# Performance work log

Measured on AMD Instinct MI355X. Metric: run time of the kernel, lower is better.

## Reference

```python
import jax, jax.numpy as jnp
import numpy as np

B, S, D_IN, E = 64, 199, 1024, 256
INNER, K = 512, 4
NH_M, DH_M = 4, 128
NH_S, DH_S = 4, 64
FF_UP = 384
SLSTM_AT = (1, 4)


def layernorm(x, w, eps=1e-5):
    mu = x.mean(-1, keepdims=True)
    var = x.var(-1, keepdims=True)
    return (x - mu) * jax.lax.rsqrt(var + eps) * w


def mh_layernorm(h, w, eps=1e-5):
    # h: (B,S,NH,DH): normalize per head over DH, scale by w (NH*DH,)
    mu = h.mean(-1, keepdims=True)
    var = h.var(-1, keepdims=True)
    hn = (h - mu) * jax.lax.rsqrt(var + eps)
    b, s, nh, dh = h.shape
    return hn.reshape(b, s, nh * dh) * w


def causal_conv(x, w, b):
    # depthwise causal conv; x (B,S,C), w (C,K), b (C,)
    k = w.shape[-1]
    s = x.shape[1]
    xp = jnp.pad(x, ((0, 0), (k - 1, 0), (0, 0)))
    y = sum(xp[:, i:i + s, :] * w[:, i] for i in range(k))
    return y + b


def headwise(x, w):
    # block-diagonal linear (LinearHeadwiseExpand): x (B,S,H*d), w (H,o,d)
    b, s, _ = x.shape
    h, o, d = w.shape
    y = jnp.einsum('bshd,hod->bsho', x.reshape(b, s, h, d), w)
    return y.reshape(b, s, h * o)


def mlstm_parallel(q, k, v, ig, fg):
    # stabilized parallel mLSTM; q,k,v (B,NH,S,DH); ig,fg (B,NH,S)
    s, dh = q.shape[2], q.shape[3]
    logf = jax.nn.log_sigmoid(fg)
    lfc = jnp.cumsum(logf, axis=-1)
    lfc = jnp.concatenate([jnp.zeros_like(lfc[..., :1]), lfc], axis=-1)  # (B,NH,S+1)
    mat = lfc[..., :, None] - lfc[..., None, :]
    mask = jnp.tril(jnp.ones((s + 1, s + 1), dtype=bool))
    mat = jnp.where(mask, mat, -jnp.inf)
    logD = mat[..., 1:, 1:] + ig[..., None, :]            # (B,NH,S,S)
    maxD = jnp.max(logD, axis=-1, keepdims=True)
    Dm = jnp.exp(logD - maxD)
    qk = jnp.einsum('bnsd,bntd->bnst', q, k) / (dh ** 0.5)
    C = qk * Dm
    norm = jnp.maximum(jnp.abs(C.sum(-1, keepdims=True)), jnp.exp(-maxD))
    return jnp.einsum('bnst,bntd->bnsd', C / (norm + 1e-6), v)


def mlstm_layer(x, proj_up, conv_w, conv_b, q_w, k_w, v_w, ig_w, ig_b, fg_w, fg_b, skip, outnorm_w, proj_down):
    b, s, _ = x.shape
    xi = x @ proj_up                                      # (B,S,2*INNER)
    x_m, z = jnp.split(xi, 2, axis=-1)
    xca = jax.nn.silu(causal_conv(x_m, conv_w, conv_b))
    q = headwise(xca, q_w)
    k = headwise(xca, k_w)
    v = headwise(x_m, v_w)
    gate_in = jnp.concatenate([q, k, v], axis=-1)         # (B,S,3*INNER)
    ig = (gate_in @ ig_w.T + ig_b).transpose(0, 2, 1)     # (B,NH,S)
    fg = (gate_in @ fg_w.T + fg_b).transpose(0, 2, 1)
    qh = q.reshape(b, s, NH_M, DH_M).transpose(0, 2, 1, 3)
    kh = k.reshape(b, s, NH_M, DH_M).transpose(0, 2, 1, 3)
    vh = v.reshape(b, s, NH_M, DH_M).transpose(0, 2, 1, 3)
    h = mlstm_parallel(qh, kh, vh, ig, fg)                # (B,NH,S,DH)
    hn = mh_layernorm(h.transpose(0, 2, 1, 3), outnorm_w) # (B,S,INNER)
    h_state = (hn + skip * xca) * jax.nn.silu(z)
    return h_state @ proj_down


def slstm_layer(x, conv_w, conv_b, gate_w, rec_w, bias, gn_w):
    b, s, _ = x.shape
    xc = jax.nn.silu(causal_conv(x, conv_w, conv_b))
    xch = xc.reshape(b, s, NH_S, DH_S)
    xh = x.reshape(b, s, NH_S, DH_S)
    gi = jnp.einsum('bshd,hod->bsho', xch, gate_w[0])
    gf = jnp.einsum('bshd,hod->bsho', xch, gate_w[1])
    gz = jnp.einsum('bshd,hod->bsho', xh, gate_w[2])
    go = jnp.einsum('bshd,hod->bsho', xh, gate_w[3])
    Wx = jnp.stack([gi, gf, gz, go], axis=2)              # (B,S,4,NH,DH)

    def step(carry, wx):
        h, c, n, m = carry
        raw = wx + jnp.einsum('bhd,ghod->bgho', h, rec_w) + bias
        iraw, fraw, zraw, oraw = raw[:, 0], raw[:, 1], raw[:, 2], raw[:, 3]
        logfplusm = m + jax.nn.log_sigmoid(fraw)
        m_new = jnp.maximum(iraw, logfplusm)
        igate = jnp.exp(iraw - m_new)
        fgate = jnp.exp(logfplusm - m_new)
        c_new = fgate * c + igate * jnp.tanh(zraw)
        n_new = fgate * n + igate
        h_new = jax.nn.sigmoid(oraw) * (c_new / n_new)
        return (h_new, c_new, n_new, m_new), h_new

    z0 = jnp.zeros((b, NH_S, DH_S), x.dtype)
    _, ys = jax.lax.scan(step, (z0, z0, z0, z0), jnp.moveaxis(Wx, 1, 0))
    y = jnp.moveaxis(ys, 0, 1)                            # (B,S,NH,DH)
    return mh_layernorm(y, gn_w)


def gated_ffn(x, w_up, w_dn):
    gate, up = jnp.split(x @ w_up, 2, axis=-1)
    return (jax.nn.gelu(gate) * up) @ w_dn


def forward_fn(x, w_down, b_down, m_ln_w, m_proj_up, m_conv_w, m_conv_b, m_q_w, m_k_w, m_v_w,
               m_ig_w, m_ig_b, m_fg_w, m_fg_b, m_skip, m_outnorm_w, m_proj_down,
               s_ln_w, s_conv_w, s_conv_b, s_gate_w, s_rec_w, s_bias, s_gn_w, s_ln2_w,
               s_ffn_up, s_ffn_down, post_ln_w, w_emo, b_emo, w_sen, b_sen):
    h = x @ w_down + b_down                               # (B,S,E)
    mi = si = 0
    for blk in range(7):
        if blk in SLSTM_AT:
            h = h + slstm_layer(layernorm(h, s_ln_w[si]), s_conv_w[si], s_conv_b[si],
                                s_gate_w[si], s_rec_w[si], s_bias[si], s_gn_w[si])
            h = h + gated_ffn(layernorm(h, s_ln2_w[si]), s_ffn_up[si], s_ffn_down[si])
            si += 1
        else:
            h = h + mlstm_layer(layernorm(h, m_ln_w[mi]), m_proj_up[mi], m_conv_w[mi], m_conv_b[mi],
                                m_q_w[mi], m_k_w[mi], m_v_w[mi], m_ig_w[mi], m_ig_b[mi],
                                m_fg_w[mi], m_fg_b[mi], m_skip[mi], m_outnorm_w[mi], m_proj_down[mi])
            mi += 1
    h = jax.nn.selu(layernorm(h, post_ln_w))
    pooled = h.mean(axis=1)                               # (B,E)
    return pooled @ w_emo + b_emo, pooled @ w_sen + b_sen


def setup_inputs() -> dict:
    ks = iter(jax.random.split(jax.random.key(0), 40))
    def p(*shape, s=0.02):
        return jax.random.normal(next(ks), shape, dtype=jnp.float32) * s
    inp = dict(
        x=jax.random.normal(next(ks), (B, S, D_IN), dtype=jnp.float32),
        w_down=p(D_IN, E), b_down=jnp.zeros((E,), jnp.float32),
        m_ln_w=jnp.ones((5, E), jnp.float32),
        m_proj_up=p(5, E, 2 * INNER),
        m_conv_w=p(5, INNER, K), m_conv_b=jnp.zeros((5, INNER), jnp.float32),
        m_q_w=p(5, 128, 4, 4), m_k_w=p(5, 128, 4, 4), m_v_w=p(5, 128, 4, 4),
        m_ig_w=p(5, NH_M, 3 * INNER), m_ig_b=p(5, NH_M, s=0.1),
        m_fg_w=p(5, NH_M, 3 * INNER),
        m_fg_b=jnp.tile(jnp.linspace(3.0, 6.0, NH_M, dtype=jnp.float32), (5, 1)),
        m_skip=jnp.ones((5, INNER), jnp.float32),
        m_outnorm_w=jnp.ones((5, INNER), jnp.float32),
        m_proj_down=p(5, INNER, E),
        s_ln_w=jnp.ones((2, E), jnp.float32),
        s_conv_w=p(2, E, K), s_conv_b=jnp.zeros((2, E), jnp.float32),
        s_gate_w=p(2, 4, NH_S, DH_S, DH_S),
        s_rec_w=p(2, 4, NH_S, DH_S, DH_S),
        s_bias=jnp.zeros((2, 4, NH_S, DH_S), jnp.float32).at[:, 1].set(3.0),
        s_gn_w=jnp.ones((2, E), jnp.float32),
        s_ln2_w=jnp.ones((2, E), jnp.float32),
        s_ffn_up=p(2, E, 2 * FF_UP), s_ffn_down=p(2, FF_UP, E),
        post_ln_w=jnp.ones((E,), jnp.float32),
        w_emo=p(E, 7), b_emo=jnp.zeros((7,), jnp.float32),
        w_sen=p(E, 3), b_sen=jnp.zeros((3,), jnp.float32),
    )
    return inp


def reference(x, w_down, b_down, m_ln_w, m_proj_up, m_conv_w, m_conv_b, m_q_w, m_k_w, m_v_w,
              m_ig_w, m_ig_b, m_fg_w, m_fg_b, m_skip, m_outnorm_w, m_proj_down,
              s_ln_w, s_conv_w, s_conv_b, s_gate_w, s_rec_w, s_bias, s_gn_w, s_ln2_w,
              s_ffn_up, s_ffn_down, post_ln_w, w_emo, b_emo, w_sen, b_sen):
    return forward_fn(x, w_down, b_down, m_ln_w, m_proj_up, m_conv_w, m_conv_b, m_q_w, m_k_w, m_v_w,
                      m_ig_w, m_ig_b, m_fg_w, m_fg_b, m_skip, m_outnorm_w, m_proj_down,
                      s_ln_w, s_conv_w, s_conv_b, s_gate_w, s_rec_w, s_bias, s_gn_w, s_ln2_w,
                      s_ffn_up, s_ffn_down, post_ln_w, w_emo, b_emo, w_sen, b_sen)
```

## Files before the change

### kernel.cpp

```cpp
#include <hip/hip_runtime.h>
#include <hip/hip_bf16.h>
#include <math.h>


#define B_    64
#define S_    199
#define E_    256
#define NTOK  (B_*S_)
#define NQT   13

typedef __attribute__((ext_vector_type(8))) short short8;
typedef __attribute__((ext_vector_type(4))) float floatx4;
typedef unsigned short ushort_t;

__device__ __forceinline__ float sigmoidf_(float x) { return 1.f / (1.f + expf(-x)); }
__device__ __forceinline__ float siluf_(float x) { return x / (1.f + expf(-x)); }
__device__ __forceinline__ float logsigf_(float x) { return fminf(x, 0.f) - log1pf(expf(-fabsf(x))); }

__device__ __forceinline__ ushort_t f2b(float f) {
    union { float f; unsigned u; } v; v.f = f;
    unsigned r = (v.u + 0x7fffu + ((v.u >> 16) & 1u)) >> 16;
    return (ushort_t)r;
}
__device__ __forceinline__ float bf2f(ushort_t u) {
    union { unsigned u; float f; } v; v.u = ((unsigned)u) << 16;
    return v.f;
}

__global__ void cvt_all(const float* __restrict__ pu, const float* __restrict__ pd,
                        const float* __restrict__ fu, const float* __restrict__ fd,
                        ushort_t* __restrict__ out, int n4) {
    int i = blockIdx.x * 256 + threadIdx.x;
    if (i >= n4) return;
    int e = i * 4;
    const float* src;
    if (e < 1310720)      src = pu + e;
    else if (e < 1966080) src = pd + (e - 1310720);
    else if (e < 2359296) src = fu + (e - 1966080);
    else                  src = fd + (e - 2359296);
    float4 v = *(const float4*)src;
    union { ushort_t us[4]; uint2 u; } t;
    t.us[0] = f2b(v.x); t.us[1] = f2b(v.y); t.us[2] = f2b(v.z); t.us[3] = f2b(v.w);
    *(uint2*)&out[e] = t.u;
}

__global__ void __launch_bounds__(256)
gemm_bf(const ushort_t* __restrict__ A, const ushort_t* __restrict__ Bw,
        const float* __restrict__ bias, float* __restrict__ C,
        int M, int K, int N, int accum) {
    __shared__ __align__(16) ushort_t As[64][40];
    __shared__ __align__(16) ushort_t Bs[128][40];
    int tid = threadIdx.x;
    int wave = tid >> 6, lane = tid & 63;
    int wm = wave >> 1, wn = wave & 1;
    int quad = lane >> 4, l16 = lane & 15;
    int m0 = blockIdx.y * 64, n0 = blockIdx.x * 128;
    floatx4 zero = {0.f, 0.f, 0.f, 0.f};
    floatx4 acc[2][4];
    #pragma unroll
    for (int i = 0; i < 2; i++)
        #pragma unroll
        for (int j = 0; j < 4; j++) acc[i][j] = zero;
    int ar = tid >> 2, ac = (tid & 3) * 8;
    int bn = tid & 127, bkg = (tid >> 7) * 16;
    for (int k0 = 0; k0 < K; k0 += 32) {
        *(uint4*)&As[ar][ac] = *(const uint4*)(A + (size_t)(m0 + ar) * K + k0 + ac);
        {
            const ushort_t* bp = Bw + (size_t)(k0 + bkg) * N + n0 + bn;
            union { ushort_t us[16]; uint4 v[2]; } t;
            #pragma unroll
            for (int i = 0; i < 16; i++) t.us[i] = bp[(size_t)i * N];
            *(uint4*)&Bs[bn][bkg] = t.v[0];
            *(uint4*)&Bs[bn][bkg + 8] = t.v[1];
        }
        __syncthreads();
        short8 af[2], bf[4];
        #pragma unroll
        for (int i = 0; i < 2; i++) af[i] = *(const short8*)&As[wm * 32 + i * 16 + l16][quad * 8];
        #pragma unroll
        for (int j = 0; j < 4; j++) bf[j] = *(const short8*)&Bs[wn * 64 + j * 16 + l16][quad * 8];
        #pragma unroll
        for (int i = 0; i < 2; i++)
            #pragma unroll
            for (int j = 0; j < 4; j++)
                acc[i][j] = __builtin_amdgcn_mfma_f32_16x16x32_bf16(af[i], bf[j], acc[i][j], 0, 0, 0);
        __syncthreads();
    }
    #pragma unroll
    for (int i = 0; i < 2; i++)
        #pragma unroll
        for (int j = 0; j < 4; j++)
            #pragma unroll
            for (int r = 0; r < 4; r++) {
                int row = m0 + wm * 32 + i * 16 + quad * 4 + r;
                int col = n0 + wn * 64 + j * 16 + l16;
                float o = acc[i][j][r];
                if (bias) o += bias[col];
                float* cp = &C[(size_t)row * N + col];
                if (accum) o += *cp;
                *cp = o;
            }
}

__global__ void __launch_bounds__(256)
gemm_mfma(const float* __restrict__ A, const float* __restrict__ Bw,
          const float* __restrict__ bias, float* __restrict__ C,
          int M, int K, int N, int accum) {
    __shared__ __align__(16) ushort_t As[64][40];
    __shared__ __align__(16) ushort_t Bs[64][40];
    int tid = threadIdx.x;
    int wave = tid >> 6, lane = tid & 63;
    int wm = wave >> 1, wn = wave & 1;
    int quad = lane >> 4, l16 = lane & 15;
    int m0 = blockIdx.y * 64, n0 = blockIdx.x * 64;
    floatx4 zero = {0.f, 0.f, 0.f, 0.f};
    floatx4 acc[2][2];
    acc[0][0] = zero; acc[0][1] = zero; acc[1][0] = zero; acc[1][1] = zero;
    int ar = tid >> 2, ac = (tid & 3) * 8;
    int bn = tid & 63, bk = (tid >> 6) * 8;
    for (int k0 = 0; k0 < K; k0 += 32) {
        {
            const float* ap = A + (size_t)(m0 + ar) * K + k0 + ac;
            union { ushort_t us[8]; uint4 v; } t;
            #pragma unroll
            for (int i = 0; i < 8; i++) t.us[i] = f2b(ap[i]);
            *(uint4*)&As[ar][ac] = t.v;
        }
        {
            const float* bp = Bw + (size_t)(k0 + bk) * N + n0 + bn;
            union { ushort_t us[8]; uint4 v; } t;
            #pragma unroll
            for (int i = 0; i < 8; i++) t.us[i] = f2b(bp[(size_t)i * N]);
            *(uint4*)&Bs[bn][bk] = t.v;
        }
        __syncthreads();
        short8 af[2], bf[2];
        #pragma unroll
        for (int i = 0; i < 2; i++) af[i] = *(const short8*)&As[wm * 32 + i * 16 + l16][quad * 8];
        #pragma unroll
        for (int j = 0; j < 2; j++) bf[j] = *(const short8*)&Bs[wn * 32 + j * 16 + l16][quad * 8];
        #pragma unroll
        for (int i = 0; i < 2; i++)
            #pragma unroll
            for (int j = 0; j < 2; j++)
                acc[i][j] = __builtin_amdgcn_mfma_f32_16x16x32_bf16(af[i], bf[j], acc[i][j], 0, 0, 0);
        __syncthreads();
    }
    #pragma unroll
    for (int i = 0; i < 2; i++)
        #pragma unroll
        for (int j = 0; j < 2; j++)
            #pragma unroll
            for (int r = 0; r < 4; r++) {
                int row = m0 + wm * 32 + i * 16 + quad * 4 + r;
                int col = n0 + wn * 32 + j * 16 + l16;
                float o = acc[i][j][r];
                if (bias) o += bias[col];
                float* cp = &C[(size_t)row * N + col];
                if (accum) o += *cp;
                *cp = o;
            }
}

__global__ void __launch_bounds__(256)
slstm_wx_mfma(const ushort_t* __restrict__ xc, const ushort_t* __restrict__ xln,
              const float* __restrict__ gw, float* __restrict__ Wx) {
    __shared__ __align__(16) ushort_t As[64][40];
    __shared__ __align__(16) ushort_t Bs[64][40];
    int gh = blockIdx.y; int g = gh >> 2, hh = gh & 3;
    const ushort_t* src = (g < 2) ? xc : xln;
    const float* w = gw + (size_t)gh * 4096;
    int tid = threadIdx.x;
    int wave = tid >> 6, lane = tid & 63;
    int wm = wave >> 1, wn = wave & 1;
    int quad = lane >> 4, l16 = lane & 15;
    int m0 = blockIdx.x * 64;
    floatx4 zero = {0.f, 0.f, 0.f, 0.f};
    floatx4 acc[2][2];
    acc[0][0] = zero; acc[0][1] = zero; acc[1][0] = zero; acc[1][1] = zero;
    int ar = tid >> 2, ac = (tid & 3) * 8;
    int bn = tid & 63, bk = (tid >> 6) * 8;
    #pragma unroll
    for (int kt = 0; kt < 2; kt++) {
        int k0 = kt * 32;
        *(uint4*)&As[ar][ac] = *(const uint4*)(src + (size_t)(m0 + ar) * 256 + hh * 64 + k0 + ac);
        {
            const float* bp = w + (size_t)bn * 64 + k0 + bk;
            union { ushort_t us[8]; uint4 v; } t;
            #pragma unroll
            for (int i = 0; i < 8; i++) t.us[i] = f2b(bp[i]);
            *(uint4*)&Bs[bn][bk] = t.v;
        }
        __syncthreads();
        short8 af[2], bf[2];
        #pragma unroll
        for (int i = 0; i < 2; i++) af[i] = *(const short8*)&As[wm * 32 + i * 16 + l16][quad * 8];
        #pragma unroll
        for (int j = 0; j < 2; j++) bf[j] = *(const short8*)&Bs[wn * 32 + j * 16 + l16][quad * 8];
        #pragma unroll
        for (int i = 0; i < 2; i++)
            #pragma unroll
            for (int j = 0; j < 2; j++)
                acc[i][j] = __builtin_amdgcn_mfma_f32_16x16x32_bf16(af[i], bf[j], acc[i][j], 0, 0, 0);
        __syncthreads();
    }
    #pragma unroll
    for (int i = 0; i < 2; i++)
        #pragma unroll
        for (int j = 0; j < 2; j++)
            #pragma unroll
            for (int r = 0; r < 4; r++) {
                int row = m0 + wm * 32 + i * 16 + quad * 4 + r;
                int col = wn * 32 + j * 16 + l16;
                Wx[(size_t)row * 1024 + g * 256 + hh * 64 + col] = acc[i][j][r];
            }
}

__global__ void __launch_bounds__(256)
layernorm256(const float* __restrict__ x, const float* __restrict__ w, ushort_t* __restrict__ y) {
    int n = blockIdx.x, t = threadIdx.x;
    float v = x[(size_t)n * 256 + t];
    float s = v, s2 = v * v;
    #pragma unroll
    for (int off = 32; off; off >>= 1) { s += __shfl_xor(s, off); s2 += __shfl_xor(s2, off); }
    __shared__ float ps[4], ps2[4];
    if ((t & 63) == 0) { ps[t >> 6] = s; ps2[t >> 6] = s2; }
    __syncthreads();
    float S = ps[0] + ps[1] + ps[2] + ps[3];
    float S2 = ps2[0] + ps2[1] + ps2[2] + ps2[3];
    float mu = S / 256.f, var = S2 / 256.f - mu * mu;
    y[(size_t)n * 256 + t] = f2b((v - mu) * rsqrtf(var + 1e-5f) * w[t]);
}

__global__ void __launch_bounds__(256)
postln_selu(const float* __restrict__ x, const float* __restrict__ w, float* __restrict__ y) {
    int n = blockIdx.x, t = threadIdx.x;
    float v = x[(size_t)n * 256 + t];
    float s = v, s2 = v * v;
    #pragma unroll
    for (int off = 32; off; off >>= 1) { s += __shfl_xor(s, off); s2 += __shfl_xor(s2, off); }
    __shared__ float ps[4], ps2[4];
    if ((t & 63) == 0) { ps[t >> 6] = s; ps2[t >> 6] = s2; }
    __syncthreads();
    float S = ps[0] + ps[1] + ps[2] + ps[3];
    float S2 = ps2[0] + ps2[1] + ps2[2] + ps2[3];
    float mu = S / 256.f, var = S2 / 256.f - mu * mu;
    float yn = (v - mu) * rsqrtf(var + 1e-5f) * w[t];
    y[(size_t)n * 256 + t] = 1.0507009873554805f * (yn > 0.f ? yn : 1.6732632423543772f * (expf(yn) - 1.f));
}

__global__ void __launch_bounds__(256)
fused_qkv(const float* __restrict__ xi, const float* __restrict__ cw,
          const float* __restrict__ cb,
          const float* __restrict__ qw, const float* __restrict__ kw,
          const float* __restrict__ vw,
          const float* __restrict__ igw, const float* __restrict__ igbias,
          const float* __restrict__ fgw, const float* __restrict__ fgbias,
          float* __restrict__ xca,
          ushort_t* __restrict__ q16, ushort_t* __restrict__ k16, ushort_t* __restrict__ v16,
          float* __restrict__ igo, float* __restrict__ fgo) {
    __shared__ float gpart[4][8];
    int tid = threadIdx.x;
    int idx = blockIdx.x * 256 + tid;
    int n = idx >> 7, hh = idx & 127;
    int b = n / S_, s = n - b * S_;
    int c0 = hh * 4;
    float4 hist[4];
    #pragma unroll
    for (int i = 0; i < 4; i++) {
        int sp = s - 3 + i;
        if (sp >= 0) hist[i] = *(const float4*)(xi + (size_t)(b * S_ + sp) * 1024 + c0);
        else hist[i] = (float4){0.f, 0.f, 0.f, 0.f};
    }
    float xm[4] = {hist[3].x, hist[3].y, hist[3].z, hist[3].w};
    float xc4[4];
    #pragma unroll
    for (int d = 0; d < 4; d++) {
        float y = cb[c0 + d];
        const float* cwp = cw + (c0 + d) * 4;
        float hv[4] = { d==0?hist[0].x:(d==1?hist[0].y:(d==2?hist[0].z:hist[0].w)),
                        d==0?hist[1].x:(d==1?hist[1].y:(d==2?hist[1].z:hist[1].w)),
                        d==0?hist[2].x:(d==1?hist[2].y:(d==2?hist[2].z:hist[2].w)),
                        xm[d] };
        #pragma unroll
        for (int i = 0; i < 4; i++) y += hv[i] * cwp[i];
        xc4[d] = siluf_(y);
    }
    *(float4*)(xca + (size_t)n * 512 + c0) = (float4){xc4[0], xc4[1], xc4[2], xc4[3]};
    float aq[4], ak[4], av[4];
    union { ushort_t us[4]; uint2 u; } qo, ko, vo;
    #pragma unroll
    for (int o = 0; o < 4; o++) {
        const float* qp = qw + (c0 + o) * 4;
        const float* kp = kw + (c0 + o) * 4;
        const float* vp = vw + (c0 + o) * 4;
        float q = 0.f, k = 0.f, v = 0.f;
        #pragma unroll
        for (int d = 0; d < 4; d++) {
            q += xc4[d] * qp[d];
            k += xc4[d] * kp[d];
            v += xm[d] * vp[d];
        }
        aq[o] = q; ak[o] = k; av[o] = v;
        qo.us[o] = f2b(q); ko.us[o] = f2b(k); vo.us[o] = f2b(v);
    }
    *(uint2*)(q16 + (size_t)n * 512 + c0) = qo.u;
    *(uint2*)(k16 + (size_t)n * 512 + c0) = ko.u;
    *(uint2*)(v16 + (size_t)n * 512 + c0) = vo.u;
    float gacc[8];
    #pragma unroll
    for (int hd = 0; hd < 4; hd++)
        #pragma unroll
        for (int wh = 0; wh < 2; wh++) {
            const float* w = (wh ? fgw : igw) + hd * 1536 + c0;
            float4 wq = *(const float4*)w;
            float4 wk = *(const float4*)(w + 512);
            float4 wv = *(const float4*)(w + 1024);
            float a = aq[0]*wq.x + aq[1]*wq.y + aq[2]*wq.z + aq[3]*wq.w
                    + ak[0]*wk.x + ak[1]*wk.y + ak[2]*wk.z + ak[3]*wk.w
                    + av[0]*wv.x + av[1]*wv.y + av[2]*wv.z + av[3]*wv.w;
            gacc[hd * 2 + wh] = a;
        }
    int lane = tid & 63, wave = tid >> 6;
    #pragma unroll
    for (int j = 0; j < 8; j++) {
        float a = gacc[j];
        #pragma unroll
        for (int off = 32; off; off >>= 1) a += __shfl_xor(a, off);
        if (lane == 0) gpart[wave][j] = a;
    }
    __syncthreads();
    if (tid < 16) {
        int token = tid >> 3, j = tid & 7;
        int hd = j >> 1, wh = j & 1;
        float val = gpart[token * 2][j] + gpart[token * 2 + 1][j]
                  + (wh ? fgbias : igbias)[hd];
        int nn = blockIdx.x * 2 + token;
        (wh ? fgo : igo)[(size_t)nn * 4 + hd] = val;
    }
}

__global__ void __launch_bounds__(256, 1)
mlstm_attn_mfma(const ushort_t* __restrict__ qb, const ushort_t* __restrict__ kb, const ushort_t* __restrict__ vb,
                const float* __restrict__ igo, const float* __restrict__ fgo,
                float* __restrict__ outb) {
    __shared__ __align__(16) ushort_t Kb[64 * 136];
    __shared__ __align__(16) ushort_t Vt[128 * 72];
    __shared__ __align__(16) ushort_t Pw[4][16 * 72];
    __shared__ float gv[208], lfv[208], mxv[208];
    int bh = blockIdx.x; int b = bh >> 2, h = bh & 3;
    int tid = threadIdx.x, wave = tid >> 6, lane = tid & 63;
    int quad = lane >> 4, l16 = lane & 15;
    if (tid < 64) {
        float vloc[4], ggl[4], gml[4], lf1[4];
        float lsum = 0.f;
        #pragma unroll
        for (int i = 0; i < 4; i++) {
            int s = tid * 4 + i;
            float f = (s < S_) ? fgo[(size_t)(b * S_ + s) * 4 + h] : 0.f;
            lsum += logsigf_(f);
            vloc[i] = lsum;
        }
        float x = lsum;
        #pragma unroll
        for (int off = 1; off < 64; off <<= 1) {
            float y = __shfl_up(x, off);
            if (tid >= off) x += y;
        }
        float excl = x - lsum;
        #pragma unroll
        for (int i = 0; i < 4; i++) lf1[i] = excl + vloc[i];
        float lmax = -1e30f;
        #pragma unroll
        for (int i = 0; i < 4; i++) {
            int s = tid * 4 + i;
            float ig_ = (s < S_) ? igo[(size_t)(b * S_ + s) * 4 + h] : -1e30f;
            ggl[i] = ig_ - lf1[i];
            lmax = fmaxf(lmax, ggl[i]);
            gml[i] = lmax;
        }
        float xm = lmax;
        #pragma unroll
        for (int off = 1; off < 64; off <<= 1) {
            float y = __shfl_up(xm, off);
            if (tid >= off) xm = fmaxf(xm, y);
        }
        float exclm = __shfl_up(xm, 1);
        if (tid == 0) exclm = -1e30f;
        #pragma unroll
        for (int i = 0; i < 4; i++) {
            int s = tid * 4 + i;
            if (s < 208) {
                if (s < S_) {
                    lfv[s] = lf1[i];
                    gv[s] = ggl[i];
                    mxv[s] = fmaxf(exclm, gml[i]);
                } else { lfv[s] = 0.f; gv[s] = 0.f; mxv[s] = 0.f; }
            }
        }
    }
    floatx4 zero = {0.f, 0.f, 0.f, 0.f};
    float rs[4][4];
    floatx4 accv[4][8];
    #pragma unroll
    for (int qi = 0; qi < 4; qi++) {
        #pragma unroll
        for (int r = 0; r < 4; r++) rs[qi][r] = 0.f;
        #pragma unroll
        for (int dt = 0; dt < 8; dt++) accv[qi][dt] = zero;
    }
    const float scale = 0.08838834764831845f;
    int trow = tid >> 4, d0 = (tid & 15) * 8;
    for (int c = 0; c < 4; c++) {
        __syncthreads();
        #pragma unroll
        for (int i = 0; i < 4; i++) {
            int tl = trow + 16 * i;
            int t = c * 64 + tl;
            union { ushort_t us[8]; uint4 v; } kk, vv;
            if (t < S_) {
                kk.v = *(const uint4*)(kb + (size_t)(b * S_ + t) * 512 + h * 128 + d0);
                vv.v = *(const uint4*)(vb + (size_t)(b * S_ + t) * 512 + h * 128 + d0);
            } else {
                kk.v = (uint4){0, 0, 0, 0};
                vv.v = (uint4){0, 0, 0, 0};
            }
            *(uint4*)&Kb[tl * 136 + d0] = kk.v;
            #pragma unroll
            for (int ii = 0; ii < 8; ii++) Vt[(d0 + ii) * 72 + tl] = vv.us[ii];
        }
        __syncthreads();
        for (int qi = 0; qi < 4; qi++) {
            int qt = wave + 4 * qi;
            if (qt >= NQT || qt < 4 * c) continue;
            uint4 z4 = {0, 0, 0, 0};
            for (int z = lane; z < 144; z += 64) ((uint4*)Pw[wave])[z] = z4;
            int srow = qt * 16 + l16;
            const ushort_t* qp = qb + (size_t)(b * S_ + min(srow, S_ - 1)) * 512 + h * 128 + quad * 8;
            short8 af[4];
            #pragma unroll
            for (int ks = 0; ks < 4; ks++) af[ks] = *(const short8*)(qp + 32 * ks);
            int ktmax_l = min(qt, 4 * c + 3) - 4 * c;
            for (int ktl = 0; ktl <= ktmax_l; ktl++) {
                floatx4 acc = zero;
                #pragma unroll
                for (int ks = 0; ks < 4; ks++) {
                    short8 bf = *(const short8*)&Kb[(ktl * 16 + l16) * 136 + quad * 8 + 32 * ks];
                    acc = __builtin_amdgcn_mfma_f32_16x16x32_bf16(af[ks], bf, acc, 0, 0, 0);
                }
                int tcol = c * 64 + ktl * 16 + l16;
                float gt = gv[tcol];
                #pragma unroll
                for (int r = 0; r < 4; r++) {
                    int s = qt * 16 + quad * 4 + r;
                    bool valid = (tcol <= s) && (tcol < S_);
                    float w = valid ? expf(gt - mxv[s]) : 0.f;
                    float p = acc[r] * scale * w;
                    rs[qi][r] += p;
                    Pw[wave][(quad * 4 + r) * 72 + ktl * 16 + l16] = f2b(p);
                }
            }
            #pragma unroll
            for (int dt = 0; dt < 8; dt++) {
                floatx4 a = accv[qi][dt];
                #pragma unroll
                for (int ks = 0; ks < 2; ks++) {
                    short8 ap = *(const short8*)&Pw[wave][l16 * 72 + quad * 8 + 32 * ks];
                    short8 bp = *(const short8*)&Vt[(dt * 16 + l16) * 72 + quad * 8 + 32 * ks];
                    a = __builtin_amdgcn_mfma_f32_16x16x32_bf16(ap, bp, a, 0, 0, 0);
                }
                accv[qi][dt] = a;
            }
        }
    }
    for (int qi = 0; qi < 4; qi++) {
        int qt = wave + 4 * qi;
        if (qt >= NQT) continue;
        float nrm[4];
        #pragma unroll
        for (int r = 0; r < 4; r++) {
            float v = rs[qi][r];
            v += __shfl_xor(v, 1); v += __shfl_xor(v, 2);
            v += __shfl_xor(v, 4); v += __shfl_xor(v, 8);
            int s = qt * 16 + quad * 4 + r;
            nrm[r] = fmaxf(fabsf(v), expf(-(lfv[s] + mxv[s]))) + 1e-6f;
        }
        #pragma unroll
        for (int dt = 0; dt < 8; dt++)
            #pragma unroll
            for (int r = 0; r < 4; r++) {
                int s = qt * 16 + quad * 4 + r;
                if (s < S_)
                    outb[(size_t)(b * S_ + s) * 512 + h * 128 + dt * 16 + l16] = accv[qi][dt][r] / nrm[r];
            }
    }
}

__global__ void __launch_bounds__(512)
mhln_hstate(const float* __restrict__ hatt, const float* __restrict__ w,
            const float* __restrict__ xca, const float* __restrict__ xi,
            const float* __restrict__ skip, ushort_t* __restrict__ out16) {
    int n = blockIdx.x, t = threadIdx.x;
    float v = hatt[(size_t)n * 512 + t];
    float s = v, s2 = v * v;
    #pragma unroll
    for (int off = 32; off; off >>= 1) { s += __shfl_xor(s, off); s2 += __shfl_xor(s2, off); }
    __shared__ float ps[8], ps2[8];
    if ((t & 63) == 0) { ps[t >> 6] = s; ps2[t >> 6] = s2; }
    __syncthreads();
    int hd = t >> 7;
    float S = ps[hd * 2] + ps[hd * 2 + 1], S2 = ps2[hd * 2] + ps2[hd * 2 + 1];
    float mu = S / 128.f, var = S2 / 128.f - mu * mu;
    float hn = (v - mu) * rsqrtf(var + 1e-5f) * w[t];
    float z = xi[(size_t)n * 1024 + 512 + t];
    out16[(size_t)n * 512 + t] = f2b((hn + skip[t] * xca[(size_t)n * 512 + t]) * siluf_(z));
}

__global__ void conv_silu_s(const ushort_t* __restrict__ xln, const float* __restrict__ cw,
                            const float* __restrict__ cb, ushort_t* __restrict__ xc) {
    int idx = blockIdx.x * blockDim.x + threadIdx.x;
    if (idx >= NTOK * 256) return;
    int n = idx >> 8, c = idx & 255;
    int b = n / S_, s = n - b * S_;
    float y = cb[c];
    #pragma unroll
    for (int i = 0; i < 4; i++) {
        int sp = s - 3 + i;
        if (sp >= 0) y += bf2f(xln[(size_t)(b * S_ + sp) * 256 + c]) * cw[c * 4 + i];
    }
    xc[idx] = f2b(siluf_(y));
}

__global__ void __launch_bounds__(256)
slstm_rec(const float* __restrict__ Wx, const float* __restrict__ rw,
          const float* __restrict__ bias, float* __restrict__ ys) {
    __shared__ __align__(16) float wl[256][68];
    __shared__ __align__(16) float hs[64];
    __shared__ float raws[4][64];
    int b = blockIdx.x >> 2, h = blockIdx.x & 3;
    int tid = threadIdx.x;
    int g = tid >> 6, o = tid & 63;
    const float* wp = rw + (size_t)(((g * 4 + h) * 64 + o)) * 64;
    #pragma unroll
    for (int i = 0; i < 16; i++) *(float4*)&wl[tid][i * 4] = *(const float4*)&wp[i * 4];
    float bi = bias[(g * 4 + h) * 64 + o];
    if (tid < 64) hs[tid] = 0.f;
    float c_ = 0.f, n_ = 0.f, m_ = 0.f;
    size_t wxbase = (size_t)(b * S_) * 1024 + g * 256 + h * 64 + o;
    float wx_cur = Wx[wxbase];
    __syncthreads();
    for (int s = 0; s < S_; s++) {
        float wx_next = (s + 1 < S_) ? Wx[wxbase + (size_t)(s + 1) * 1024] : 0.f;
        float a0 = 0.f, a1 = 0.f, a2 = 0.f, a3 = 0.f;
        #pragma unroll
        for (int d4 = 0; d4 < 16; d4++) {
            float4 wv = *(const float4*)&wl[tid][d4 * 4];
            float4 hv = *(const float4*)&hs[d4 * 4];
            a0 += hv.x * wv.x;
            a1 += hv.y * wv.y;
            a2 += hv.z * wv.z;
            a3 += hv.w * wv.w;
        }
        raws[g][o] = (a0 + a1) + (a2 + a3) + wx_cur + bi;
        __syncthreads();
        float ir = raws[0][o], fr = raws[1][o], zr = raws[2][o], orr = raws[3][o];
        float lfpm = m_ + logsigf_(fr);
        float mn = fmaxf(ir, lfpm);
        float ig = expf(ir - mn), fg = expf(lfpm - mn);
        c_ = fg * c_ + ig * tanhf(zr);
        n_ = fg * n_ + ig;
        m_ = mn;
        float hn = sigmoidf_(orr) * (c_ / n_);
        if (g == 0) {
            hs[o] = hn;
            ys[(size_t)(b * S_ + s) * 256 + h * 64 + o] = hn;
        }
        __syncthreads();
        wx_cur = wx_next;
    }
}

__global__ void __launch_bounds__(256)
slstm_post(const float* __restrict__ ys, const float* __restrict__ gn_w,
           float* __restrict__ h, const float* __restrict__ ln2_w,
           ushort_t* __restrict__ ln16) {
    int n = blockIdx.x, t = threadIdx.x;
    float v = ys[(size_t)n * 256 + t];
    float s = v, s2 = v * v;
    #pragma unroll
    for (int off = 32; off; off >>= 1) { s += __shfl_xor(s, off); s2 += __shfl_xor(s2, off); }
    float mu = s / 64.f, var = s2 / 64.f - mu * mu;
    float hv = h[(size_t)n * 256 + t] + (v - mu) * rsqrtf(var + 1e-5f) * gn_w[t];
    h[(size_t)n * 256 + t] = hv;
    float S = hv, S2 = hv * hv;
    #pragma unroll
    for (int off = 32; off; off >>= 1) { S += __shfl_xor(S, off); S2 += __shfl_xor(S2, off); }
    __shared__ float ps[4], ps2[4];
    if ((t & 63) == 0) { ps[t >> 6] = S; ps2[t >> 6] = S2; }
    __syncthreads();
    float St = ps[0] + ps[1] + ps[2] + ps[3];
    float S2t = ps2[0] + ps2[1] + ps2[2] + ps2[3];
    float mu2 = St / 256.f, var2 = S2t / 256.f - mu2 * mu2;
    ln16[(size_t)n * 256 + t] = f2b((hv - mu2) * rsqrtf(var2 + 1e-5f) * ln2_w[t]);
}

__global__ void ffn_act(const float* __restrict__ up, ushort_t* __restrict__ act) {
    int idx = blockIdx.x * blockDim.x + threadIdx.x;
    if (idx >= NTOK * 384) return;
    int n = idx / 384, j = idx - n * 384;
    float g = up[(size_t)n * 768 + j], u = up[(size_t)n * 768 + 384 + j];
    float t = tanhf(0.7978845608028654f * (g + 0.044715f * g * g * g));
    act[idx] = f2b(0.5f * g * (1.f + t) * u);
}

__global__ void pool_k(const float* __restrict__ a, float* __restrict__ pooled) {
    int b = blockIdx.x, e = threadIdx.x;
    float s = 0.f;
    for (int t = 0; t < S_; t++) s += a[(size_t)(b * S_ + t) * 256 + e];
    pooled[b * 256 + e] = s / (float)S_;
}

__global__ void heads_k(const float* __restrict__ pooled,
                        const float* __restrict__ we, const float* __restrict__ be,
                        const float* __restrict__ ws, const float* __restrict__ bs,
                        float* __restrict__ out) {
    int i = blockIdx.x * blockDim.x + threadIdx.x;
    if (i < B_ * 7) {
        int b = i / 7, o = i - b * 7;
        float a = be[o];
        for (int e = 0; e < 256; e++) a += pooled[b * 256 + e] * we[e * 7 + o];
        out[b * 7 + o] = a;
    } else if (i < B_ * 7 + B_ * 3) {
        int j = i - B_ * 7;
        int b = j / 3, o = j - b * 3;
        float a = bs[o];
        for (int e = 0; e < 256; e++) a += pooled[b * 256 + e] * ws[e * 3 + o];
        out[B_ * 7 + b * 3 + o] = a;
    }
}

extern "C" void kernel_launch(void* const* d_in, const int* in_sizes, int n_in,
                              void* d_out, int out_size, void* d_ws, size_t ws_size,
                              hipStream_t stream) {
    (void)in_sizes; (void)n_in; (void)out_size; (void)ws_size;
    const float* x          = (const float*)d_in[0];
    const float* w_down     = (const float*)d_in[1];
    const float* b_down     = (const float*)d_in[2];
    const float* m_ln_w     = (const float*)d_in[3];
    const float* m_proj_up  = (const float*)d_in[4];
    const float* m_conv_w   = (const float*)d_in[5];
    const float* m_conv_b   = (const float*)d_in[6];
    const float* m_q_w      = (const float*)d_in[7];
    const float* m_k_w      = (const float*)d_in[8];
    const float* m_v_w      = (const float*)d_in[9];
    const float* m_ig_w     = (const float*)d_in[10];
    const float* m_ig_b     = (const float*)d_in[11];
    const float* m_fg_w     = (const float*)d_in[12];
    const float* m_fg_b     = (const float*)d_in[13];
    const float* m_skip     = (const float*)d_in[14];
    const float* m_outnorm  = (const float*)d_in[15];
    const float* m_proj_dn  = (const float*)d_in[16];
    const float* s_ln_w     = (const float*)d_in[17];
    const float* s_conv_w   = (const float*)d_in[18];
    const float* s_conv_b   = (const float*)d_in[19];
    const float* s_gate_w   = (const float*)d_in[20];
    const float* s_rec_w    = (const float*)d_in[21];
    const float* s_bias     = (const float*)d_in[22];
    const float* s_gn_w     = (const float*)d_in[23];
    const float* s_ln2_w    = (const float*)d_in[24];
    const float* s_ffn_up   = (const float*)d_in[25];
    const float* s_ffn_dn   = (const float*)d_in[26];
    const float* post_ln_w  = (const float*)d_in[27];
    const float* w_emo      = (const float*)d_in[28];
    const float* b_emo      = (const float*)d_in[29];
    const float* w_sen      = (const float*)d_in[30];
    const float* b_sen      = (const float*)d_in[31];

    float* W    = (float*)d_ws;
    float* h    = W;
    float* lnb  = h    + (size_t)NTOK * 256;
    float* big0 = lnb  + (size_t)NTOK * 256;
    float* xca  = big0 + (size_t)NTOK * 1024;
    float* qb   = xca  + (size_t)NTOK * 512;
    float* kb   = qb   + (size_t)NTOK * 512;
    float* vb   = kb   + (size_t)NTOK * 512;
    float* hatt = vb   + (size_t)NTOK * 512;
    float* igo  = hatt + (size_t)NTOK * 512;
    float* fgo  = igo  + (size_t)NTOK * 4;
    float* lfcb = fgo  + (size_t)NTOK * 4;
    float* Mxb  = lfcb + (size_t)256 * (S_ + 1);
    float* pooled = Mxb + (size_t)256 * S_;
    ushort_t* lnb16 = (ushort_t*)lnb;
    ushort_t* qb16  = (ushort_t*)qb;
    ushort_t* kb16  = (ushort_t*)kb;
    ushort_t* vb16  = (ushort_t*)vb;
    ushort_t* hat16 = qb16 + (size_t)NTOK * 512;
    ushort_t* xc16  = (ushort_t*)(vb16 + (size_t)NTOK * 512);
    ushort_t* wpk   = (ushort_t*)(pooled + 64 * 256);
    ushort_t* wp_pu = wpk;
    ushort_t* wp_pd = wp_pu + 5 * 262144;
    ushort_t* wp_fu = wp_pd + 5 * 131072;
    ushort_t* wp_fd = wp_fu + 2 * 196608;

    cvt_all<<<(638976 + 255) / 256, 256, 0, stream>>>(m_proj_up, m_proj_dn, s_ffn_up, s_ffn_dn, wpk, 638976);

    gemm_mfma<<<dim3(256 / 64, NTOK / 64), 256, 0, stream>>>(x, w_down, b_down, h, NTOK, 1024, 256, 0);

    int mi = 0, si = 0;
    for (int blk = 0; blk < 7; blk++) {
        if (blk == 1 || blk == 4) {
            layernorm256<<<NTOK, 256, 0, stream>>>(h, s_ln_w + si * 256, lnb16);
            conv_silu_s<<<(NTOK * 256 + 255) / 256, 256, 0, stream>>>(lnb16, s_conv_w + si * 1024, s_conv_b + si * 256, xc16);
            slstm_wx_mfma<<<dim3(NTOK / 64, 16), 256, 0, stream>>>(xc16, lnb16, s_gate_w + (size_t)si * 65536, big0);
            slstm_rec<<<256, 256, 0, stream>>>(big0, s_rec_w + (size_t)si * 65536, s_bias + si * 1024, hatt);
            slstm_post<<<NTOK, 256, 0, stream>>>(hatt, s_gn_w + si * 256, h, s_ln2_w + si * 256, lnb16);
            gemm_bf<<<dim3(768 / 128, NTOK / 64), 256, 0, stream>>>(lnb16, wp_fu + (size_t)si * 196608, nullptr, big0, NTOK, 256, 768, 0);
            ffn_act<<<(NTOK * 384 + 255) / 256, 256, 0, stream>>>(big0, hat16);
            gemm_bf<<<dim3(256 / 128, NTOK / 64), 256, 0, stream>>>(hat16, wp_fd + (size_t)si * 98304, nullptr, h, NTOK, 384, 256, 1);
            si++;
        } else {
            layernorm256<<<NTOK, 256, 0, stream>>>(h, m_ln_w + mi * 256, lnb16);
            gemm_bf<<<dim3(1024 / 128, NTOK / 64), 256, 0, stream>>>(lnb16, wp_pu + (size_t)mi * 262144, nullptr, big0, NTOK, 256, 1024, 0);
            fused_qkv<<<NTOK / 2, 256, 0, stream>>>(big0, m_conv_w + mi * 2048, m_conv_b + mi * 512,
                                                    m_q_w + mi * 2048, m_k_w + mi * 2048, m_v_w + mi * 2048,
                                                    m_ig_w + mi * 6144, m_ig_b + mi * 4,
                                                    m_fg_w + mi * 6144, m_fg_b + mi * 4,
                                                    xca, qb16, kb16, vb16, igo, fgo);
            mlstm_attn_mfma<<<256, 256, 0, stream>>>(qb16, kb16, vb16, igo, fgo, hatt);
            mhln_hstate<<<NTOK, 512, 0, stream>>>(hatt, m_outnorm + mi * 512, xca, big0, m_skip + mi * 512, hat16);
            gemm_bf<<<dim3(256 / 128, NTOK / 64), 256, 0, stream>>>(hat16, wp_pd + (size_t)mi * 131072, nullptr, h, NTOK, 512, 256, 1);
            mi++;
        }
    }

    postln_selu<<<NTOK, 256, 0, stream>>>(h, post_ln_w, xca);
    pool_k<<<B_, 256, 0, stream>>>(xca, pooled);
    heads_k<<<3, 256, 0, stream>>>(pooled, w_emo, b_emo, w_sen, b_sen, (float*)d_out);
}
```

Before: 1.979 ms.

## Batch sLSTM recurrence over 16 sequences per block with bf16 MFMA

The sLSTM recurrent kernel used to give each block one (batch, head) pair and compute a 64x64 matvec per gate in fp32 from LDS, with two barriers per timestep. It now gives each block one head and 16 batch rows. The recurrent weights sit in registers as bf16 MFMA fragments, the hidden state is double-buffered in LDS as bf16, and each step needs one barrier. This raises per-step compute density and halves the barriers, at the cost of launching only 16 blocks (lower parallelism) and rounding the recurrent state to bf16, which may hurt accuracy.

```diff
diff --git a/kernel.cpp b/kernel.cpp
--- a/kernel.cpp
+++ b/kernel.cpp
@@ -25,6 +25,12 @@
 __device__ __forceinline__ float bf2f(ushort_t u) {
     union { unsigned u; float f; } v; v.u = ((unsigned)u) << 16;
     return v.f;
+}
+__device__ __forceinline__ short8 cvt8(const float* p) {
+    union { ushort_t us[8]; short8 v; } t;
+    #pragma unroll
+    for (int i = 0; i < 8; i++) t.us[i] = f2b(p[i]);
+    return t.v;
 }
 
 __global__ void cvt_all(const float* __restrict__ pu, const float* __restrict__ pd,
@@ -531,52 +537,82 @@
     xc[idx] = f2b(siluf_(y));
 }
 
-__global__ void __launch_bounds__(256)
+__global__ void __launch_bounds__(256, 1)
 slstm_rec(const float* __restrict__ Wx, const float* __restrict__ rw,
           const float* __restrict__ bias, float* __restrict__ ys) {
-    __shared__ __align__(16) float wl[256][68];
-    __shared__ __align__(16) float hs[64];
-    __shared__ float raws[4][64];
-    int b = blockIdx.x >> 2, h = blockIdx.x & 3;
+    __shared__ __align__(16) ushort_t hsb[2][16][72];
+    int h = blockIdx.x >> 2;
+    int bbase = (blockIdx.x & 3) * 16;
     int tid = threadIdx.x;
-    int g = tid >> 6, o = tid & 63;
-    const float* wp = rw + (size_t)(((g * 4 + h) * 64 + o)) * 64;
-    #pragma unroll
-    for (int i = 0; i < 16; i++) *(float4*)&wl[tid][i * 4] = *(const float4*)&wp[i * 4];
-    float bi = bias[(g * 4 + h) * 64 + o];
-    if (tid < 64) hs[tid] = 0.f;
-    float c_ = 0.f, n_ = 0.f, m_ = 0.f;
-    size_t wxbase = (size_t)(b * S_) * 1024 + g * 256 + h * 64 + o;
-    float wx_cur = Wx[wxbase];
+    int w = tid >> 6, lane = tid & 63;
+    int quad = lane >> 4, l16 = lane & 15;
+    int d = w * 16 + l16;
+    short8 bfr[4][2];
+    #pragma unroll
+    for (int g = 0; g < 4; g++)
+        #pragma unroll
+        for (int ks = 0; ks < 2; ks++)
+            bfr[g][ks] = cvt8(rw + (size_t)((g * 4 + h) * 64 + d) * 64 + ks * 32 + quad * 8);
+    float bi[4];
+    #pragma unroll
+    for (int g = 0; g < 4; g++) bi[g] = bias[(g * 4 + h) * 64 + d];
+    float c_[4] = {0.f, 0.f, 0.f, 0.f};
+    float n_[4] = {0.f, 0.f, 0.f, 0.f};
+    float m_[4] = {0.f, 0.f, 0.f, 0.f};
+    size_t wxb[4], ysb[4];
+    #pragma unroll
+    for (int r = 0; r < 4; r++) {
+        int bb = bbase + quad * 4 + r;
+        wxb[r] = (size_t)(bb * S_) * 1024 + h * 64 + d;
+        ysb[r] = (size_t)(bb * S_) * 256 + h * 64 + d;
+    }
+    for (int i = tid; i < 16 * 72; i += 256) ((ushort_t*)hsb[0])[i] = 0;
+    float wxc[4][4];
+    #pragma unroll
+    for (int g = 0; g < 4; g++)
+        #pragma unroll
+        for (int r = 0; r < 4; r++)
+            wxc[g][r] = Wx[wxb[r] + g * 256];
     __syncthreads();
+    int pb = 0;
     for (int s = 0; s < S_; s++) {
-        float wx_next = (s + 1 < S_) ? Wx[wxbase + (size_t)(s + 1) * 1024] : 0.f;
-        float a0 = 0.f, a1 = 0.f, a2 = 0.f, a3 = 0.f;
-        #pragma unroll
-        for (int d4 = 0; d4 < 16; d4++) {
-            float4 wv = *(const float4*)&wl[tid][d4 * 4];
-            float4 hv = *(const float4*)&hs[d4 * 4];
-            a0 += hv.x * wv.x;
-            a1 += hv.y * wv.y;
-            a2 += hv.z * wv.z;
-            a3 += hv.w * wv.w;
-        }
-        raws[g][o] = (a0 + a1) + (a2 + a3) + wx_cur + bi;
-        __syncthreads();
-        float ir = raws[0][o], fr = raws[1][o], zr = raws[2][o], orr = raws[3][o];
-        float lfpm = m_ + logsigf_(fr);
-        float mn = fmaxf(ir, lfpm);
-        float ig = expf(ir - mn), fg = expf(lfpm - mn);
-        c_ = fg * c_ + ig * tanhf(zr);
-        n_ = fg * n_ + ig;
-        m_ = mn;
-        float hn = sigmoidf_(orr) * (c_ / n_);
-        if (g == 0) {
-            hs[o] = hn;
-            ys[(size_t)(b * S_ + s) * 256 + h * 64 + o] = hn;
-        }
-        __syncthreads();
-        wx_cur = wx_next;
+        short8 a0 = *(const short8*)&hsb[pb][l16][quad * 8];
+        short8 a1 = *(const short8*)&hsb[pb][l16][quad * 8 + 32];
+        floatx4 acc[4];
+        #pragma unroll
+        for (int g = 0; g < 4; g++) {
+            acc[g][0] = wxc[g][0] + bi[g];
+            acc[g][1] = wxc[g][1] + bi[g];
+            acc[g][2] = wxc[g][2] + bi[g];
+            acc[g][3] = wxc[g][3] + bi[g];
+        }
+        if (s + 1 < S_) {
+            #pragma unroll
+            for (int g = 0; g < 4; g++)
+                #pragma unroll
+                for (int r = 0; r < 4; r++)
+                    wxc[g][r] = Wx[wxb[r] + (size_t)(s + 1) * 1024 + g * 256];
+        }
+        #pragma unroll
+        for (int g = 0; g < 4; g++) {
+            acc[g] = __builtin_amdgcn_mfma_f32_16x16x32_bf16(a0, bfr[g][0], acc[g], 0, 0, 0);
+            acc[g] = __builtin_amdgcn_mfma_f32_16x16x32_bf16(a1, bfr[g][1], acc[g], 0, 0, 0);
+        }
+        #pragma unroll
+        for (int r = 0; r < 4; r++) {
+            float ir = acc[0][r], fr = acc[1][r], zr = acc[2][r], orr = acc[3][r];
+            float lfpm = m_[r] + logsigf_(fr);
+            float mn = fmaxf(ir, lfpm);
+            float ig = expf(ir - mn), fg = expf(lfpm - mn);
+            c_[r] = fg * c_[r] + ig * tanhf(zr);
+            n_[r] = fg * n_[r] + ig;
+            m_[r] = mn;
+            float hn = sigmoidf_(orr) * (c_[r] / n_[r]);
+            hsb[pb ^ 1][quad * 4 + r][d] = f2b(hn);
+            ys[ysb[r] + (size_t)s * 256] = hn;
+        }
+        __syncthreads();
+        pb ^= 1;
     }
 }
 
@@ -712,7 +748,7 @@
             layernorm256<<<NTOK, 256, 0, stream>>>(h, s_ln_w + si * 256, lnb16);
             conv_silu_s<<<(NTOK * 256 + 255) / 256, 256, 0, stream>>>(lnb16, s_conv_w + si * 1024, s_conv_b + si * 256, xc16);
             slstm_wx_mfma<<<dim3(NTOK / 64, 16), 256, 0, stream>>>(xc16, lnb16, s_gate_w + (size_t)si * 65536, big0);
-            slstm_rec<<<256, 256, 0, stream>>>(big0, s_rec_w + (size_t)si * 65536, s_bias + si * 1024, hatt);
+            slstm_rec<<<16, 256, 0, stream>>>(big0, s_rec_w + (size_t)si * 65536, s_bias + si * 1024, hatt);
             slstm_post<<<NTOK, 256, 0, stream>>>(hatt, s_gn_w + si * 256, h, s_ln2_w + si * 256, lnb16);
             gemm_bf<<<dim3(768 / 128, NTOK / 64), 256, 0, stream>>>(lnb16, wp_fu + (size_t)si * 196608, nullptr, big0, NTOK, 256, 768, 0);
             ffn_act<<<(NTOK * 384 + 255) / 256, 256, 0, stream>>>(big0, hat16);
```

Result: slower. 2.384 ms (+20.5%).
